# Performance work log

Hardware: AMD Instinct MI355X
Metric: run time of the kernel (lower is better)

The kernel has to match this reference:

```python
import jax, jax.numpy as jnp
import numpy as np

IN_FEATURES = 1024
OUT_FEATURES = 1024
DEGREE = 8
BATCH = 8192


def setup_inputs() -> dict:
    key = jax.random.key(0)
    kx, kc = jax.random.split(key)
    x = jax.random.normal(kx, (BATCH, IN_FEATURES), dtype=jnp.float32)
    std = 1.0 / (IN_FEATURES * (DEGREE + 1))
    coefficients = std * jax.random.normal(
        kc, (IN_FEATURES, OUT_FEATURES, DEGREE + 1), dtype=jnp.float32)
    return {"x": x, "coefficients": coefficients}


def reference(x, coefficients):
    # x: (B, I); coefficients: (I, O, D+1)
    t = jnp.tanh(x)
    # Chebyshev recursion T_0=1, T_1=t, T_k = 2 t T_{k-1} - T_{k-2}
    vals = [jnp.ones_like(t), t]
    for _ in range(2, DEGREE + 1):
        vals.append(2.0 * t * vals[-1] - vals[-2])
    cheby = jnp.stack(vals, axis=-1)  # (B, I, D+1)
    return jnp.einsum('bid,iod->bo', cheby, coefficients)
```

## Files before the change

### kernel.cpp

```cpp
#include <hip/hip_runtime.h>
#include <hip/hip_bf16.h>
#include <stdint.h>

#define BATCH 8192
#define INF   1024
#define GN    1024
#define GK    8192

#define BM 256
#define BN 128
#define BK 64
#define NT (GK / BK)
#define ABYTES (BM * BK * 2)
#define BBYTES (BN * BK * 2)
#define BUFSZ  (ABYTES + BBYTES)
#define SMEM_BYTES (3 * BUFSZ)

typedef __attribute__((ext_vector_type(4))) float floatx4;
typedef __attribute__((ext_vector_type(8))) short short8;

static __device__ __forceinline__ ushort f2bf(float f) {
  union { float f; uint32_t u; } v; v.f = f;
  uint32_t r = v.u + 0x7FFF + ((v.u >> 16) & 1);
  return (ushort)(r >> 16);
}

__global__ __launch_bounds__(256) void repack(const float* __restrict__ coef,
                                              ushort* __restrict__ Wt,
                                              float* __restrict__ bias) {
  __shared__ ushort lds[32 * 9 * 33];
  __shared__ float  bl[32 * 33];
  const int i0 = (blockIdx.x >> 5) << 5;
  const int o0 = (blockIdx.x & 31) << 5;
  const int t = threadIdx.x;
  for (int idx = t; idx < 32 * 288; idx += 256) {
    const int ii  = idx / 288;
    const int rem = idx - ii * 288;
    const float f = coef[(size_t)(i0 + ii) * 9216 + (size_t)o0 * 9 + rem];
    lds[rem * 33 + ii] = f2bf(f);
    const int oo = rem / 9;
    if (rem == oo * 9) bl[oo * 33 + ii] = f;
  }
  __syncthreads();
  if (t < 32) {
    float s = 0.f;
    #pragma unroll
    for (int ii = 0; ii < 32; ++ii) s += bl[t * 33 + ii];
    atomicAdd(&bias[o0 + t], s);
  }
  for (int idx = t; idx < 32 * 8 * 32; idx += 256) {
    const int oo  = idx >> 8;
    const int rem = idx & 255;
    const int d1  = rem >> 5;
    const int ii  = rem & 31;
    Wt[(size_t)(o0 + oo) * GK + (size_t)d1 * 1024 + (i0 + ii)] =
        lds[(oo * 9 + d1 + 1) * 33 + ii];
  }
}

__global__ __launch_bounds__(256) void featurize(const float* __restrict__ x,
                                                 ushort* __restrict__ Cf) {
  const int tid = blockIdx.x * 256 + threadIdx.x;
  const size_t idx4 = (size_t)tid << 2;
  const int b = tid >> 8;
  const int i = (tid & 255) << 2;
  const float4 v = *reinterpret_cast<const float4*>(x + idx4);
  float t[4] = {tanhf(v.x), tanhf(v.y), tanhf(v.z), tanhf(v.w)};
  float Tp[4] = {1.f, 1.f, 1.f, 1.f};
  float Tc[4] = {t[0], t[1], t[2], t[3]};
  ushort* base = Cf + (size_t)b * GK + i;
  #pragma unroll
  for (int d = 1; d <= 8; ++d) {
    ushort4 u;
    u.x = f2bf(Tc[0]); u.y = f2bf(Tc[1]); u.z = f2bf(Tc[2]); u.w = f2bf(Tc[3]);
    *reinterpret_cast<ushort4*>(base + (size_t)(d - 1) * 1024) = u;
    #pragma unroll
    for (int j = 0; j < 4; ++j) {
      const float Tn = 2.f * t[j] * Tc[j] - Tp[j];
      Tp[j] = Tc[j]; Tc[j] = Tn;
    }
  }
}


__device__ __forceinline__ void gload16(const char* src, char* dstp) {
  __builtin_amdgcn_global_load_lds(
      (const __attribute__((address_space(1))) void*)src,
      (__attribute__((address_space(3))) void*)dstp, 16, 0, 0);
}

template<int CB, int NB, bool DOSTAGE, bool VM6>
__device__ __forceinline__ void tile_step(char* smem, int kt,
    const char* const* gA, const char* const* gB, int dst,
    int wm0, int wn0, int lr, int lk, floatx4 (&acc)[4][4]) {
  const char* Ab = smem + CB * BUFSZ;
  const char* Bb = smem + CB * BUFSZ + ABYTES;
  const int xm = lr & 7;
  const size_t kb = (size_t)(kt + 2) * 128;
  short8 af[4][2], bf[4][2];

#define QUAD(MI0, NI0)                                                         \
  __builtin_amdgcn_s_setprio(1);                                               \
  _Pragma("unroll") for (int kk = 0; kk < 2; ++kk)                             \
    _Pragma("unroll") for (int mi = MI0; mi < MI0 + 2; ++mi)                   \
      _Pragma("unroll") for (int ni = NI0; ni < NI0 + 2; ++ni)                 \
        acc[mi][ni] = __builtin_amdgcn_mfma_f32_16x16x32_bf16(                 \
            af[mi][kk], bf[ni][kk], acc[mi][ni], 0, 0, 0);                     \
  __builtin_amdgcn_s_setprio(0);

  #pragma unroll
  for (int mi = 0; mi < 2; ++mi)
    #pragma unroll
    for (int kk = 0; kk < 2; ++kk)
      af[mi][kk] = *reinterpret_cast<const short8*>(
          Ab + (wm0 + mi * 16 + lr) * 128 + ((((kk << 2) | lk) ^ xm) << 4));
  #pragma unroll
  for (int ni = 0; ni < 2; ++ni)
    #pragma unroll
    for (int kk = 0; kk < 2; ++kk)
      bf[ni][kk] = *reinterpret_cast<const short8*>(
          Bb + (wn0 + ni * 16 + lr) * 128 + ((((kk << 2) | lk) ^ xm) << 4));
  if (DOSTAGE) {
    gload16(gA[0] + kb, smem + NB * BUFSZ + 0 * 8192 + dst);
    gload16(gA[1] + kb, smem + NB * BUFSZ + 1 * 8192 + dst);
  }
  __builtin_amdgcn_s_barrier();
  __builtin_amdgcn_sched_barrier(0);
  QUAD(0, 0)

  #pragma unroll
  for (int mi = 2; mi < 4; ++mi)
    #pragma unroll
    for (int kk = 0; kk < 2; ++kk)
      af[mi][kk] = *reinterpret_cast<const short8*>(
          Ab + (wm0 + mi * 16 + lr) * 128 + ((((kk << 2) | lk) ^ xm) << 4));
  #pragma unroll
  for (int ni = 2; ni < 4; ++ni)
    #pragma unroll
    for (int kk = 0; kk < 2; ++kk)
      bf[ni][kk] = *reinterpret_cast<const short8*>(
          Bb + (wn0 + ni * 16 + lr) * 128 + ((((kk << 2) | lk) ^ xm) << 4));
  if (DOSTAGE) {
    gload16(gA[2] + kb, smem + NB * BUFSZ + 2 * 8192 + dst);
    gload16(gA[3] + kb, smem + NB * BUFSZ + 3 * 8192 + dst);
  }
  __builtin_amdgcn_s_barrier();
  __builtin_amdgcn_sched_barrier(0);
  QUAD(0, 2)

  if (DOSTAGE) {
    gload16(gB[0] + kb, smem + NB * BUFSZ + ABYTES + 0 * 8192 + dst);
    gload16(gB[1] + kb, smem + NB * BUFSZ + ABYTES + 1 * 8192 + dst);
  }
  __builtin_amdgcn_s_barrier();
  __builtin_amdgcn_sched_barrier(0);
  QUAD(2, 0)

  if (VM6) asm volatile("s_waitcnt vmcnt(6)" ::: "memory");
  else     asm volatile("s_waitcnt vmcnt(0)" ::: "memory");
  __builtin_amdgcn_s_barrier();
  __builtin_amdgcn_sched_barrier(0);
  QUAD(2, 2)
#undef QUAD
}

__global__ __launch_bounds__(512, 2) void gemm_bt(const ushort* __restrict__ A,
                                                  const ushort* __restrict__ Bt,
                                                  const float* __restrict__ bias,
                                                  float* __restrict__ C) {
  extern __shared__ __align__(16) char smem[];
  const int t = threadIdx.x;
  const int bid = (blockIdx.x & 7) * 32 + (blockIdx.x >> 3);
  const int bm0 = (bid >> 3) << 8;
  const int bn0 = (bid & 7) << 7;
  const int lane = t & 63;
  const int wid  = t >> 6;
  const int wm0 = (wid >> 1) << 6;
  const int wn0 = (wid & 1) << 6;
  const int lr = lane & 15;
  const int lk = lane >> 4;

  const int srow = t >> 3;
  const int schunk = ((t & 7) ^ (srow & 7)) << 4;
  const char* gA[4]; const char* gB[2];
  #pragma unroll
  for (int j = 0; j < 4; ++j)
    gA[j] = (const char*)(A + (size_t)(bm0 + j * 64 + srow) * GK) + schunk;
  #pragma unroll
  for (int j = 0; j < 2; ++j)
    gB[j] = (const char*)(Bt + (size_t)(bn0 + j * 64 + srow) * GK) + schunk;
  const int dst = t << 4;

  floatx4 acc[4][4] = {};

  #pragma unroll
  for (int j = 0; j < 4; ++j) gload16(gA[j], smem + j * 8192 + dst);
  #pragma unroll
  for (int j = 0; j < 2; ++j) gload16(gB[j], smem + ABYTES + j * 8192 + dst);
  #pragma unroll
  for (int j = 0; j < 4; ++j) gload16(gA[j] + 128, smem + BUFSZ + j * 8192 + dst);
  #pragma unroll
  for (int j = 0; j < 2; ++j) gload16(gB[j] + 128, smem + BUFSZ + ABYTES + j * 8192 + dst);
  asm volatile("s_waitcnt vmcnt(6)" ::: "memory");
  __builtin_amdgcn_s_barrier();
  __builtin_amdgcn_sched_barrier(0);

  for (int kt = 0; kt < NT - 2; kt += 3) {
    tile_step<0, 2, true, true>(smem, kt,     gA, gB, dst, wm0, wn0, lr, lk, acc);
    tile_step<1, 0, true, true>(smem, kt + 1, gA, gB, dst, wm0, wn0, lr, lk, acc);
    tile_step<2, 1, true, true>(smem, kt + 2, gA, gB, dst, wm0, wn0, lr, lk, acc);
  }
  tile_step<0, 2, false, false>(smem, 126, gA, gB, dst, wm0, wn0, lr, lk, acc);
  tile_step<1, 0, false, false>(smem, 127, gA, gB, dst, wm0, wn0, lr, lk, acc);

  #pragma unroll
  for (int ni = 0; ni < 4; ++ni) {
    const int col = bn0 + wn0 + ni * 16 + lr;
    const float bv = bias[col];
    #pragma unroll
    for (int mi = 0; mi < 4; ++mi) {
      const int row = bm0 + wm0 + mi * 16 + lk * 4;
      #pragma unroll
      for (int r = 0; r < 4; ++r)
        C[(size_t)(row + r) * GN + col] = acc[mi][ni][r] + bv;
    }
  }
}

extern "C" void kernel_launch(void* const* d_in, const int* in_sizes, int n_in,
                              void* d_out, int out_size, void* d_ws, size_t ws_size,
                              hipStream_t stream) {
  const float* x    = (const float*)d_in[0];
  const float* coef = (const float*)d_in[1];
  float* out = (float*)d_out;

  char* ws = (char*)d_ws;
  ushort* Cf   = (ushort*)ws;
  ushort* Wt   = (ushort*)(ws + (size_t)BATCH * GK * 2);
  float*  bias = (float*)(ws + (size_t)BATCH * GK * 2 + (size_t)GN * GK * 2);

  hipFuncSetAttribute(reinterpret_cast<const void*>(&gemm_bt),
                      hipFuncAttributeMaxDynamicSharedMemorySize, SMEM_BYTES);

  hipMemsetAsync(bias, 0, GN * sizeof(float), stream);
  repack<<<1024, 256, 0, stream>>>(coef, Wt, bias);
  featurize<<<(BATCH * INF / 4) / 256, 256, 0, stream>>>(x, Cf);
  gemm_bt<<<256, 512, SMEM_BYTES, stream>>>(Cf, Wt, bias, out);
}
```

Before: 248.7 us.

## Load B fragments directly from global into registers, drop B from LDS

```diff
diff --git a/kernel.cpp b/kernel.cpp
--- a/kernel.cpp
+++ b/kernel.cpp
@@ -12,9 +12,7 @@
 #define BK 64
 #define NT (GK / BK)
 #define ABYTES (BM * BK * 2)
-#define BBYTES (BN * BK * 2)
-#define BUFSZ  (ABYTES + BBYTES)
-#define SMEM_BYTES (3 * BUFSZ)
+#define SMEM_BYTES (3 * ABYTES)
 
 typedef __attribute__((ext_vector_type(4))) float floatx4;
 typedef __attribute__((ext_vector_type(8))) short short8;
@@ -61,22 +59,26 @@
 __global__ __launch_bounds__(256) void featurize(const float* __restrict__ x,
                                                  ushort* __restrict__ Cf) {
   const int tid = blockIdx.x * 256 + threadIdx.x;
-  const size_t idx4 = (size_t)tid << 2;
-  const int b = tid >> 8;
-  const int i = (tid & 255) << 2;
-  const float4 v = *reinterpret_cast<const float4*>(x + idx4);
-  float t[4] = {tanhf(v.x), tanhf(v.y), tanhf(v.z), tanhf(v.w)};
-  float Tp[4] = {1.f, 1.f, 1.f, 1.f};
-  float Tc[4] = {t[0], t[1], t[2], t[3]};
+  const int b = tid >> 7;
+  const int i = (tid & 127) << 3;
+  const float* xp = x + (size_t)b * INF + i;
+  const float4 v0 = *reinterpret_cast<const float4*>(xp);
+  const float4 v1 = *reinterpret_cast<const float4*>(xp + 4);
+  float tt[8] = {tanhf(v0.x), tanhf(v0.y), tanhf(v0.z), tanhf(v0.w),
+                 tanhf(v1.x), tanhf(v1.y), tanhf(v1.z), tanhf(v1.w)};
+  float Tp[8], Tc[8];
+  #pragma unroll
+  for (int j = 0; j < 8; ++j) { Tp[j] = 1.f; Tc[j] = tt[j]; }
   ushort* base = Cf + (size_t)b * GK + i;
   #pragma unroll
   for (int d = 1; d <= 8; ++d) {
-    ushort4 u;
-    u.x = f2bf(Tc[0]); u.y = f2bf(Tc[1]); u.z = f2bf(Tc[2]); u.w = f2bf(Tc[3]);
-    *reinterpret_cast<ushort4*>(base + (size_t)(d - 1) * 1024) = u;
-    #pragma unroll
-    for (int j = 0; j < 4; ++j) {
-      const float Tn = 2.f * t[j] * Tc[j] - Tp[j];
+    short8 u;
+    #pragma unroll
+    for (int j = 0; j < 8; ++j) u[j] = (short)f2bf(Tc[j]);
+    *reinterpret_cast<short8*>(base + (size_t)(d - 1) * 1024) = u;
+    #pragma unroll
+    for (int j = 0; j < 8; ++j) {
+      const float Tn = 2.f * tt[j] * Tc[j] - Tp[j];
       Tp[j] = Tc[j]; Tc[j] = Tn;
     }
   }
@@ -89,15 +91,16 @@
       (__attribute__((address_space(3))) void*)dstp, 16, 0, 0);
 }
 
-template<int CB, int NB, bool DOSTAGE, bool VM6>
+template<int CB, bool DOSTAGE, bool PFB, int VMN>
 __device__ __forceinline__ void tile_step(char* smem, int kt,
-    const char* const* gA, const char* const* gB, int dst,
-    int wm0, int wn0, int lr, int lk, floatx4 (&acc)[4][4]) {
-  const char* Ab = smem + CB * BUFSZ;
-  const char* Bb = smem + CB * BUFSZ + ABYTES;
+    const char* const* gA, const char* const* gBf, int dst,
+    int wm0, int lr, int lk,
+    short8 (&bfu)[4][2], short8 (&bff)[4][2], floatx4 (&acc)[4][4]) {
+  constexpr int NB = (CB + 2) % 3;
+  const char* Ab = smem + CB * ABYTES;
   const int xm = lr & 7;
   const size_t kb = (size_t)(kt + 2) * 128;
-  short8 af[4][2], bf[4][2];
+  short8 af[4][2];
 
 #define QUAD(MI0, NI0)                                                         \
   __builtin_amdgcn_s_setprio(1);                                               \
@@ -105,24 +108,26 @@
     _Pragma("unroll") for (int mi = MI0; mi < MI0 + 2; ++mi)                   \
       _Pragma("unroll") for (int ni = NI0; ni < NI0 + 2; ++ni)                 \
         acc[mi][ni] = __builtin_amdgcn_mfma_f32_16x16x32_bf16(                 \
-            af[mi][kk], bf[ni][kk], acc[mi][ni], 0, 0, 0);                     \
+            af[mi][kk], bfu[ni][kk], acc[mi][ni], 0, 0, 0);                    \
   __builtin_amdgcn_s_setprio(0);
 
+  if (PFB) {
+    const size_t koff = (size_t)(kt + 1) * 128;
+    #pragma unroll
+    for (int ni = 0; ni < 4; ++ni)
+      #pragma unroll
+      for (int kk = 0; kk < 2; ++kk)
+        bff[ni][kk] = *reinterpret_cast<const short8*>(gBf[ni] + koff + kk * 64);
+  }
   #pragma unroll
   for (int mi = 0; mi < 2; ++mi)
     #pragma unroll
     for (int kk = 0; kk < 2; ++kk)
       af[mi][kk] = *reinterpret_cast<const short8*>(
           Ab + (wm0 + mi * 16 + lr) * 128 + ((((kk << 2) | lk) ^ xm) << 4));
-  #pragma unroll
-  for (int ni = 0; ni < 2; ++ni)
-    #pragma unroll
-    for (int kk = 0; kk < 2; ++kk)
-      bf[ni][kk] = *reinterpret_cast<const short8*>(
-          Bb + (wn0 + ni * 16 + lr) * 128 + ((((kk << 2) | lk) ^ xm) << 4));
   if (DOSTAGE) {
-    gload16(gA[0] + kb, smem + NB * BUFSZ + 0 * 8192 + dst);
-    gload16(gA[1] + kb, smem + NB * BUFSZ + 1 * 8192 + dst);
+    gload16(gA[0] + kb, smem + NB * ABYTES + 0 * 8192 + dst);
+    gload16(gA[1] + kb, smem + NB * ABYTES + 1 * 8192 + dst);
   }
   __builtin_amdgcn_s_barrier();
   __builtin_amdgcn_sched_barrier(0);
@@ -134,30 +139,21 @@
     for (int kk = 0; kk < 2; ++kk)
       af[mi][kk] = *reinterpret_cast<const short8*>(
           Ab + (wm0 + mi * 16 + lr) * 128 + ((((kk << 2) | lk) ^ xm) << 4));
-  #pragma unroll
-  for (int ni = 2; ni < 4; ++ni)
-    #pragma unroll
-    for (int kk = 0; kk < 2; ++kk)
-      bf[ni][kk] = *reinterpret_cast<const short8*>(
-          Bb + (wn0 + ni * 16 + lr) * 128 + ((((kk << 2) | lk) ^ xm) << 4));
   if (DOSTAGE) {
-    gload16(gA[2] + kb, smem + NB * BUFSZ + 2 * 8192 + dst);
-    gload16(gA[3] + kb, smem + NB * BUFSZ + 3 * 8192 + dst);
+    gload16(gA[2] + kb, smem + NB * ABYTES + 2 * 8192 + dst);
+    gload16(gA[3] + kb, smem + NB * ABYTES + 3 * 8192 + dst);
   }
   __builtin_amdgcn_s_barrier();
   __builtin_amdgcn_sched_barrier(0);
   QUAD(0, 2)
 
-  if (DOSTAGE) {
-    gload16(gB[0] + kb, smem + NB * BUFSZ + ABYTES + 0 * 8192 + dst);
-    gload16(gB[1] + kb, smem + NB * BUFSZ + ABYTES + 1 * 8192 + dst);
-  }
   __builtin_amdgcn_s_barrier();
   __builtin_amdgcn_sched_barrier(0);
   QUAD(2, 0)
 
-  if (VM6) asm volatile("s_waitcnt vmcnt(6)" ::: "memory");
-  else     asm volatile("s_waitcnt vmcnt(0)" ::: "memory");
+  if constexpr (VMN == 12) asm volatile("s_waitcnt vmcnt(12)" ::: "memory");
+  else if constexpr (VMN == 8) asm volatile("s_waitcnt vmcnt(8)" ::: "memory");
+  else asm volatile("s_waitcnt vmcnt(0)" ::: "memory");
   __builtin_amdgcn_s_barrier();
   __builtin_amdgcn_sched_barrier(0);
   QUAD(2, 2)
@@ -182,36 +178,43 @@
 
   const int srow = t >> 3;
   const int schunk = ((t & 7) ^ (srow & 7)) << 4;
-  const char* gA[4]; const char* gB[2];
+  const char* gA[4];
   #pragma unroll
   for (int j = 0; j < 4; ++j)
     gA[j] = (const char*)(A + (size_t)(bm0 + j * 64 + srow) * GK) + schunk;
-  #pragma unroll
-  for (int j = 0; j < 2; ++j)
-    gB[j] = (const char*)(Bt + (size_t)(bn0 + j * 64 + srow) * GK) + schunk;
   const int dst = t << 4;
 
+  const char* gBf[4];
+  #pragma unroll
+  for (int ni = 0; ni < 4; ++ni)
+    gBf[ni] = (const char*)(Bt + (size_t)(bn0 + wn0 + ni * 16 + lr) * GK) + lk * 16;
+
   floatx4 acc[4][4] = {};
+  short8 bf0[4][2], bf1[4][2];
 
   #pragma unroll
   for (int j = 0; j < 4; ++j) gload16(gA[j], smem + j * 8192 + dst);
   #pragma unroll
-  for (int j = 0; j < 2; ++j) gload16(gB[j], smem + ABYTES + j * 8192 + dst);
-  #pragma unroll
-  for (int j = 0; j < 4; ++j) gload16(gA[j] + 128, smem + BUFSZ + j * 8192 + dst);
-  #pragma unroll
-  for (int j = 0; j < 2; ++j) gload16(gB[j] + 128, smem + BUFSZ + ABYTES + j * 8192 + dst);
-  asm volatile("s_waitcnt vmcnt(6)" ::: "memory");
-  __builtin_amdgcn_s_barrier();
-  __builtin_amdgcn_sched_barrier(0);
-
-  for (int kt = 0; kt < NT - 2; kt += 3) {
-    tile_step<0, 2, true, true>(smem, kt,     gA, gB, dst, wm0, wn0, lr, lk, acc);
-    tile_step<1, 0, true, true>(smem, kt + 1, gA, gB, dst, wm0, wn0, lr, lk, acc);
-    tile_step<2, 1, true, true>(smem, kt + 2, gA, gB, dst, wm0, wn0, lr, lk, acc);
-  }
-  tile_step<0, 2, false, false>(smem, 126, gA, gB, dst, wm0, wn0, lr, lk, acc);
-  tile_step<1, 0, false, false>(smem, 127, gA, gB, dst, wm0, wn0, lr, lk, acc);
+  for (int j = 0; j < 4; ++j) gload16(gA[j] + 128, smem + ABYTES + j * 8192 + dst);
+  #pragma unroll
+  for (int ni = 0; ni < 4; ++ni)
+    #pragma unroll
+    for (int kk = 0; kk < 2; ++kk)
+      bf0[ni][kk] = *reinterpret_cast<const short8*>(gBf[ni] + kk * 64);
+  asm volatile("s_waitcnt vmcnt(12)" ::: "memory");
+  __builtin_amdgcn_s_barrier();
+  __builtin_amdgcn_sched_barrier(0);
+
+  for (int kt = 0; kt < NT - 2; kt += 6) {
+    tile_step<0, true, true, 12>(smem, kt,     gA, gBf, dst, wm0, lr, lk, bf0, bf1, acc);
+    tile_step<1, true, true, 12>(smem, kt + 1, gA, gBf, dst, wm0, lr, lk, bf1, bf0, acc);
+    tile_step<2, true, true, 12>(smem, kt + 2, gA, gBf, dst, wm0, lr, lk, bf0, bf1, acc);
+    tile_step<0, true, true, 12>(smem, kt + 3, gA, gBf, dst, wm0, lr, lk, bf1, bf0, acc);
+    tile_step<1, true, true, 12>(smem, kt + 4, gA, gBf, dst, wm0, lr, lk, bf0, bf1, acc);
+    tile_step<2, true, true, 12>(smem, kt + 5, gA, gBf, dst, wm0, lr, lk, bf1, bf0, acc);
+  }
+  tile_step<0, false, true, 8>(smem, 126, gA, gBf, dst, wm0, lr, lk, bf0, bf1, acc);
+  tile_step<1, false, false, 0>(smem, 127, gA, gBf, dst, wm0, lr, lk, bf1, bf0, acc);
 
   #pragma unroll
   for (int ni = 0; ni < 4; ++ni) {
@@ -244,6 +247,6 @@
 
   hipMemsetAsync(bias, 0, GN * sizeof(float), stream);
   repack<<<1024, 256, 0, stream>>>(coef, Wt, bias);
-  featurize<<<(BATCH * INF / 4) / 256, 256, 0, stream>>>(x, Cf);
+  featurize<<<(BATCH * INF / 8) / 256, 256, 0, stream>>>(x, Cf);
   gemm_bt<<<256, 512, SMEM_BYTES, stream>>>(Cf, Wt, bias, out);
 }
```

Result: slower. 429.5 us (+72.7%).
